# Optimization experiments

Measured on AMD Instinct MI355X. Metric: run time of the kernel, lower is better.

Reference implementation:

```python
import jax, jax.numpy as jnp
import numpy as np

B, S, D, H = 8, 2048, 256, 4
DH = D // H
DFF = 4 * D


def setup_inputs() -> dict:
    key = jax.random.key(0)
    ks = jax.random.split(key, 32)
    w = lambda k, sh: (jax.random.normal(k, sh, jnp.float32) * 0.02)
    inp = {
        'global_feat': jax.random.normal(ks[0], (B, S, D), jnp.float32),
        'local_feat': jax.random.normal(ks[1], (B, S, D), jnp.float32),
        'text_feat': jax.random.normal(ks[2], (B, S, D), jnp.float32),
        'Wl1': w(ks[3], (D, D)), 'bl1': jnp.zeros((D,), jnp.float32),
        'Wl2': w(ks[4], (D, D)), 'bl2': jnp.zeros((D,), jnp.float32),
        'Wg': w(ks[5], (D, D)), 'bg': jnp.zeros((D,), jnp.float32),
        'Wgq': w(ks[6], (D, D)), 'bgq': jnp.zeros((D,), jnp.float32),
        'Wgk': w(ks[7], (D, D)), 'bgk': jnp.zeros((D,), jnp.float32),
        'Wgv': w(ks[8], (D, D)), 'bgv': jnp.zeros((D,), jnp.float32),
        'Wpq': w(ks[9], (D, D)), 'bpq': jnp.zeros((D,), jnp.float32),
        'Wpk': w(ks[10], (D, D)), 'bpk': jnp.zeros((D,), jnp.float32),
        'Wpv': w(ks[11], (D, D)), 'bpv': jnp.zeros((D,), jnp.float32),
        'Wd': w(ks[12], (D, D)), 'bd': jnp.zeros((D,), jnp.float32),
        'Wm1': w(ks[13], (D, DFF)), 'bm1': jnp.zeros((DFF,), jnp.float32),
        'Wm2': w(ks[14], (DFF, D)), 'bm2': jnp.zeros((D,), jnp.float32),
        'Wml': w(ks[15], (D, D)), 'bml': jnp.zeros((D,), jnp.float32),
    }
    return inp


def _heads(x):
    # [B,S,D] -> [B,H,S,DH]
    return x.reshape(B, S, H, DH).transpose(0, 2, 1, 3)


def _merge(x):
    # [B,H,S,DH] -> [B,S,D]
    return x.transpose(0, 2, 1, 3).reshape(B, S, D)


def reference(global_feat, local_feat, text_feat,
              Wl1, bl1, Wl2, bl2, Wg, bg,
              Wgq, bgq, Wgk, bgk, Wgv, bgv,
              Wpq, bpq, Wpk, bpk, Wpv, bpv,
              Wd, bd, Wm1, bm1, Wm2, bm2, Wml, bml):
    scale = 1.0 / jnp.sqrt(jnp.asarray(DH, jnp.float32))
    # embedding projections (dropout inactive in eval mode)
    dup_local = local_feat @ Wl1 + bl1      # local_embedding_1
    local = local_feat @ Wl2 + bl2          # local_embedding_2
    glob = global_feat @ Wg + bg            # global_embedding
    # global branch: Q from global, K/V from local
    gq = _heads(glob @ Wgq + bgq)
    gk = _heads(local @ Wgk + bgk)
    gv = _heads(local @ Wgv + bgv)
    # local branch: Q from duplicate local, K/V from text
    pq = _heads(dup_local @ Wpq + bpq)
    pk = _heads(text_feat @ Wpk + bpk)
    pv = _heads(text_feat @ Wpv + bpv)
    glb_probs = jax.nn.softmax(jnp.einsum('bhqd,bhkd->bhqk', gq, gk) * scale, axis=-1)
    plb_probs = jax.nn.softmax(jnp.einsum('bhqd,bhkd->bhqk', pq, pk) * scale, axis=-1)
    # bridging matmul: fuse probability maps
    plb_enhanced = jnp.einsum('bhqk,bhkl->bhql', glb_probs, plb_probs)
    glb_ctx = _merge(jnp.einsum('bhqk,bhkd->bhqd', glb_probs, gv))
    plb_ctx = _merge(jnp.einsum('bhqk,bhkd->bhqd', plb_enhanced, pv))
    out = (glb_ctx + plb_ctx) @ Wd + bd
    # GPT-style MLP (c_fc -> GELU -> c_proj)
    out = jax.nn.gelu(out @ Wm1 + bm1) @ Wm2 + bm2
    out = out @ Wml + bml
    return out
```

## Files before the change

kernel.cpp:

```cpp
#include <hip/hip_runtime.h>
#include <math.h>

#define Bn 8
#define Sn 2048
#define Dn 256
#define Hn 4
#define DHn 64
#define Mn (Bn*Sn)

typedef short bf16x8 __attribute__((ext_vector_type(8)));
typedef float f32x2  __attribute__((ext_vector_type(2)));
typedef float f32x4  __attribute__((ext_vector_type(4)));
typedef float f32x16 __attribute__((ext_vector_type(16)));
typedef int   i32x4  __attribute__((ext_vector_type(4)));
typedef unsigned short u16;
typedef unsigned int   u32;
typedef unsigned long long u64;

#if defined(__has_builtin)
#if __has_builtin(__builtin_amdgcn_global_load_lds)
#define HAVE_GLL 1
#endif
#if __has_builtin(__builtin_amdgcn_permlane32_swap)
#define HAVE_PLS 1
#endif
#endif
#ifndef HAVE_GLL
#define HAVE_GLL 0
#endif
#ifndef HAVE_PLS
#define HAVE_PLS 0
#endif

__device__ __forceinline__ u16 f2b(float f){
    u32 u = __float_as_uint(f);
    u32 r = (u + 0x7fffu + ((u >> 16) & 1u)) >> 16;
    return (u16)r;
}
__device__ __forceinline__ float b2f(u16 h){ return __uint_as_float(((u32)h) << 16); }
__device__ __forceinline__ u32 cvtpk(float lo, float hi){
    u32 r;
    asm("v_cvt_pk_bf16_f32 %0, %1, %2" : "=v"(r) : "v"(lo), "v"(hi));
    return r;
}

__device__ __forceinline__ float gelu_f(float x){
    const float K1 = 2.3021143113f;
    const float K2 = 0.1029390163f;
    float x2 = x * x;
    float arg = fmaf(x2 * x, K2, x * K1);
    float e = exp2f(arg);
    float r = __builtin_amdgcn_rcpf(e + 1.0f);
    return x - x * r;
}

struct WtArgs {
    const float* src[13];
    int kdim[13], ndim[13], dstoff[13], t0[13], rm[13];
};
struct BcArgs {
    const float* W2[4];
    const float* b1[4];
    const float* b2[4];
    int off[4];
    float* fb;
    int bc0;
};

__global__ __launch_bounds__(256) void prep_k(WtArgs a, u16* __restrict__ dst, BcArgs bc)
{
    __shared__ float tile[32][33];
    int bx = blockIdx.x;
    if (bx >= bc.bc0){
        int p = bx - bc.bc0, aa = threadIdx.x;
        const float* W2 = bc.W2[p];
        const float* b1 = bc.b1[p];
        const float* b2 = bc.b2[p];
        float s = b2[aa];
        for (int j = 0; j < 256; ++j) s = fmaf(b1[j], W2[(size_t)j*256 + aa], s);
        bc.fb[bc.off[p] + aa] = s;
        if (p == 0) bc.fb[1024 + aa] = 0.f;
        return;
    }
    int tb = bx;
    int wi = 0;
    #pragma unroll
    for (int i = 1; i < 13; ++i) if (tb >= a.t0[i]) wi = i;
    int tt = tb - a.t0[wi];
    int N = a.ndim[wi], K = a.kdim[wi];
    int ntn = N >> 5;
    int tn = tt % ntn, tk = tt / ntn;
    int n0 = tn * 32, k0 = tk * 32;
    const float* src = a.src[wi];
    u16* out = dst + a.dstoff[wi];
    int r = threadIdx.x >> 5, c = threadIdx.x & 31;
    if (a.rm[wi]){
        #pragma unroll
        for (int rr = 0; rr < 4; ++rr){
            size_t idx = (size_t)(k0 + r*4 + rr) * N + n0 + c;
            out[idx] = f2b(src[idx]);
        }
        return;
    }
    #pragma unroll
    for (int rr = 0; rr < 4; ++rr)
        tile[r*4+rr][c] = src[(size_t)(k0 + r*4 + rr) * N + n0 + c];
    __syncthreads();
    #pragma unroll
    for (int rr = 0; rr < 4; ++rr)
        out[(size_t)(n0 + r*4 + rr) * K + k0 + c] = f2b(tile[c][r*4+rr]);
}

struct Grp {
    const u16* A[6];
    const u16* Wt[6];
    const float* bias[6];
    void* C[6];
    float scale[6];
};

template<int ACT, int OUTF32>
__global__ __launch_bounds__(256, 4) void gemm_k(Grp g, int N, int K)
{
    const u32 gx = gridDim.x, gy = gridDim.y;
    const u32 lgx = (u32)__builtin_ctz(gx);
    const u32 lgy = (u32)__builtin_ctz(gy);
    const u32 total = gx * gy * gridDim.z;
    const u32 lid = (blockIdx.z * gy + blockIdx.y) * gx + blockIdx.x;
    const u32 nl = (lid & 7) * (total >> 3) + (lid >> 3);
    const u32 bz = nl >> (lgx + lgy);
    const u32 by = (nl >> lgx) & (gy - 1);
    const u32 bx = nl & (gx - 1);

    const u16* __restrict__ A   = g.A[bz];
    const u16* __restrict__ Wt  = g.Wt[bz];
    const float* __restrict__ bias = g.bias[bz];
    void* __restrict__ Cv = g.C[bz];
    const float scale = g.scale[bz];

    __shared__ u16 sm[2][6144];
    const int tid = threadIdx.x;
    const int w = tid >> 6, lane = tid & 63;
    const int l15 = lane & 15, l4 = lane >> 4;
    const int wr = w & 1, wc = w >> 1;
    const int bm = by << 6, bn = bx << 7;
    const int xq = l4 ^ ((lane >> 1) & 3);

    f32x4 acc[4][2];
    #pragma unroll
    for (int nf = 0; nf < 4; ++nf)
        #pragma unroll
        for (int mf = 0; mf < 2; ++mf){
            acc[nf][mf][0]=0.f; acc[nf][mf][1]=0.f; acc[nf][mf][2]=0.f; acc[nf][mf][3]=0.f;
        }

    auto STAGE = [&](int buf, int kt){
        #pragma unroll
        for (int j = 0; j < 3; ++j){
            int ch = w*192 + j*64 + lane;
            int isB = ch >= 256;
            int cc  = isB ? ch - 256 : ch;
            int row = cc >> 2, q = cc & 3;
            int qs  = q ^ ((row >> 1) & 3);
            const u16* src = isB ? (Wt + (size_t)(bn + row) * K + kt + qs*8)
                                 : (A  + (size_t)(bm + row) * K + kt + qs*8);
#if HAVE_GLL
            u16* lb = &sm[buf][(size_t)(w*192 + j*64) * 8];
            __builtin_amdgcn_global_load_lds((const __attribute__((address_space(1))) void*)src,
                                             (__attribute__((address_space(3))) void*)lb, 16, 0, 0);
#else
            *(i32x4*)&sm[buf][(size_t)ch * 8] = *(const i32x4*)src;
#endif
        }
    };

    STAGE(0, 0);
    const int nk = K >> 5;
    for (int t = 0; t < nk; ++t){
        const int cur = t & 1;
        if (t + 1 < nk){
            STAGE(cur ^ 1, (t + 1) << 5);
#if HAVE_GLL
            asm volatile("s_waitcnt vmcnt(3)" ::: "memory");
#endif
        } else {
#if HAVE_GLL
            asm volatile("s_waitcnt vmcnt(0)" ::: "memory");
#endif
        }
        __builtin_amdgcn_s_barrier();
        asm volatile("" ::: "memory");

        const u16* As = sm[cur];
        const u16* Bs = sm[cur] + 2048;
        bf16x8 wf[4], af[2];
        #pragma unroll
        for (int nf = 0; nf < 4; ++nf)
            wf[nf] = *(const bf16x8*)(Bs + (size_t)(wc*64 + nf*16 + l15) * 32 + xq*8);
        #pragma unroll
        for (int mf = 0; mf < 2; ++mf)
            af[mf] = *(const bf16x8*)(As + (size_t)(wr*32 + mf*16 + l15) * 32 + xq*8);
        __builtin_amdgcn_s_setprio(1);
        #pragma unroll
        for (int nf = 0; nf < 4; ++nf)
            #pragma unroll
            for (int mf = 0; mf < 2; ++mf)
                acc[nf][mf] = __builtin_amdgcn_mfma_f32_16x16x32_bf16(wf[nf], af[mf], acc[nf][mf], 0, 0, 0);
        __builtin_amdgcn_s_setprio(0);

        asm volatile("" ::: "memory");
        __builtin_amdgcn_s_barrier();
    }

    #pragma unroll
    for (int nf = 0; nf < 4; ++nf){
        const int n0 = bn + wc*64 + nf*16 + l4*4;
        float4 b4 = *(const float4*)(bias + n0);
        #pragma unroll
        for (int mf = 0; mf < 2; ++mf){
            const int m = bm + wr*32 + mf*16 + l15;
            float r0 = (acc[nf][mf][0] + b4.x) * scale;
            float r1 = (acc[nf][mf][1] + b4.y) * scale;
            float r2 = (acc[nf][mf][2] + b4.z) * scale;
            float r3 = (acc[nf][mf][3] + b4.w) * scale;
            if (ACT){ r0 = gelu_f(r0); r1 = gelu_f(r1); r2 = gelu_f(r2); r3 = gelu_f(r3); }
            if (OUTF32){
                float4 o; o.x = r0; o.y = r1; o.z = r2; o.w = r3;
                *(float4*)((float*)Cv + (size_t)m * N + n0) = o;
            } else {
                u64 p = (u64)cvtpk(r0, r1) | ((u64)cvtpk(r2, r3) << 32);
                *(u64*)((u16*)Cv + (size_t)m * N + n0) = p;
            }
        }
    }
}

struct Grp32 {
    const float* A[6];
    const u16* Wt[6];
    const float* bias[6];
    void* C[6];
    float scale[6];
};

__global__ __launch_bounds__(256, 4) void gemm32_k(Grp32 g, int N, int K)
{
    const u32 gx = gridDim.x, gy = gridDim.y;
    const u32 lgx = (u32)__builtin_ctz(gx);
    const u32 lgy = (u32)__builtin_ctz(gy);
    const u32 total = gx * gy * gridDim.z;
    const u32 lid = (blockIdx.z * gy + blockIdx.y) * gx + blockIdx.x;
    const u32 nl = (lid & 7) * (total >> 3) + (lid >> 3);
    const u32 bz = nl >> (lgx + lgy);
    const u32 by = (nl >> lgx) & (gy - 1);
    const u32 bx = nl & (gx - 1);

    const float* __restrict__ A = g.A[bz];
    const u16* __restrict__ Wt  = g.Wt[bz];
    const float* __restrict__ bias = g.bias[bz];
    void* __restrict__ Cv = g.C[bz];
    const float scale = g.scale[bz];

    __shared__ u16 sm[2][6144];
    const int tid = threadIdx.x;
    const int w = tid >> 6, lane = tid & 63;
    const int l15 = lane & 15, l4 = lane >> 4;
    const int wr = w & 1, wc = w >> 1;
    const int bm = by << 6, bn = bx << 7;
    const int xq = l4 ^ ((lane >> 1) & 3);

    f32x4 acc[4][2];
    #pragma unroll
    for (int nf = 0; nf < 4; ++nf)
        #pragma unroll
        for (int mf = 0; mf < 2; ++mf){
            acc[nf][mf][0]=0.f; acc[nf][mf][1]=0.f; acc[nf][mf][2]=0.f; acc[nf][mf][3]=0.f;
        }

    const int arow = tid >> 2, aq = tid & 3;
    const int aqs = aq ^ ((arow >> 1) & 3);
    const float* Ab = A + (size_t)(bm + arow) * K + aqs*8;
    float4 a0r, a1r;
    auto A_ISSUE = [&](int kt){
        a0r = *(const float4*)(Ab + kt);
        a1r = *(const float4*)(Ab + kt + 4);
    };
    auto A_WRITE = [&](int buf){
        i32x4 o;
        o[0] = (int)cvtpk(a0r.x, a0r.y); o[1] = (int)cvtpk(a0r.z, a0r.w);
        o[2] = (int)cvtpk(a1r.x, a1r.y); o[3] = (int)cvtpk(a1r.z, a1r.w);
        *(i32x4*)&sm[buf][(size_t)tid * 8] = o;
    };
    auto B_STAGE = [&](int buf, int kt){
        #pragma unroll
        for (int j = 0; j < 2; ++j){
            int ch = w*128 + j*64 + lane;
            int row = ch >> 2, q = ch & 3;
            int qs  = q ^ ((row >> 1) & 3);
            const u16* src = Wt + (size_t)(bn + row) * K + kt + qs*8;
#if HAVE_GLL
            u16* lb = &sm[buf][2048 + (size_t)(w*128 + j*64) * 8];
            __builtin_amdgcn_global_load_lds((const __attribute__((address_space(1))) void*)src,
                                             (__attribute__((address_space(3))) void*)lb, 16, 0, 0);
#else
            *(i32x4*)&sm[buf][2048 + (size_t)ch * 8] = *(const i32x4*)src;
#endif
        }
    };

    A_ISSUE(0);
    B_STAGE(0, 0);
    A_WRITE(0);
    __syncthreads();

    const int nk = K >> 5;
    for (int t = 0; t < nk; ++t){
        const int cur = t & 1;
        if (t + 1 < nk){
            A_ISSUE((t + 1) << 5);
            B_STAGE(cur ^ 1, (t + 1) << 5);
#if HAVE_GLL
            asm volatile("s_waitcnt vmcnt(4)" ::: "memory");
#endif
        } else {
#if HAVE_GLL
            asm volatile("s_waitcnt vmcnt(0)" ::: "memory");
#endif
        }
        __builtin_amdgcn_s_barrier();
        asm volatile("" ::: "memory");

        const u16* As = sm[cur];
        const u16* Bs = sm[cur] + 2048;
        bf16x8 wf[4], af[2];
        #pragma unroll
        for (int nf = 0; nf < 4; ++nf)
            wf[nf] = *(const bf16x8*)(Bs + (size_t)(wc*64 + nf*16 + l15) * 32 + xq*8);
        #pragma unroll
        for (int mf = 0; mf < 2; ++mf)
            af[mf] = *(const bf16x8*)(As + (size_t)(wr*32 + mf*16 + l15) * 32 + xq*8);
        __builtin_amdgcn_s_setprio(1);
        #pragma unroll
        for (int nf = 0; nf < 4; ++nf)
            #pragma unroll
            for (int mf = 0; mf < 2; ++mf)
                acc[nf][mf] = __builtin_amdgcn_mfma_f32_16x16x32_bf16(wf[nf], af[mf], acc[nf][mf], 0, 0, 0);
        __builtin_amdgcn_s_setprio(0);

        if (t + 1 < nk) A_WRITE(cur ^ 1);
        asm volatile("" ::: "memory");
        asm volatile("s_waitcnt lgkmcnt(0)" ::: "memory");
        __builtin_amdgcn_s_barrier();
    }

    #pragma unroll
    for (int nf = 0; nf < 4; ++nf){
        const int n0 = bn + wc*64 + nf*16 + l4*4;
        float4 b4 = *(const float4*)(bias + n0);
        #pragma unroll
        for (int mf = 0; mf < 2; ++mf){
            const int m = bm + wr*32 + mf*16 + l15;
            float r0 = (acc[nf][mf][0] + b4.x) * scale;
            float r1 = (acc[nf][mf][1] + b4.y) * scale;
            float r2 = (acc[nf][mf][2] + b4.z) * scale;
            float r3 = (acc[nf][mf][3] + b4.w) * scale;
            u64 p = (u64)cvtpk(r0, r1) | ((u64)cvtpk(r2, r3) << 32);
            *(u64*)((u16*)Cv + (size_t)m * N + n0) = p;
        }
    }
}

template<int FUSE>
__global__ __launch_bounds__(256, 2) void attn_k(const u16* __restrict__ Q, const u16* __restrict__ Kp,
                                                 const u16* __restrict__ Vp, u16* __restrict__ O,
                                                 const u16* __restrict__ ADD)
{
    __shared__ u16 Kl[2][2][4608];
    __shared__ u16 Vt[2][2][4608];

    const int tid = threadIdx.x;
    const int w = tid >> 6, lane = tid & 63;
    const int c31 = lane & 31, h = lane >> 5;

    const int lid = blockIdx.x;
    const int nl = (lid & 7) * 64 + (lid >> 3);
    const int bh = nl >> 4;
    const int qb = (nl & 15) << 7;
    const size_t hb = (size_t)(bh >> 2) * Sn * Dn + (size_t)(bh & 3) * DHn;
    const int qrow = qb + w*32 + c31;

    bf16x8 qf[4];
    #pragma unroll
    for (int kc = 0; kc < 4; ++kc)
        qf[kc] = *(const bf16x8*)(Q + hb + (size_t)qrow * Dn + kc*16 + h*8);

    f32x16 ot0, ot1;
    #pragma unroll
    for (int r = 0; r < 16; ++r){ ot0[r] = 0.f; ot1[r] = 0.f; }
    float ll = 0.f;

    int koff0[4], koff1[4];
    #pragma unroll
    for (int kc = 0; kc < 4; ++kc){
        koff0[kc] = c31*72        + kc*16 + h*8;
        koff1[kc] = (32 + c31)*72 + kc*16 + h*8;
    }

    const int krow = tid >> 1, kq = (tid & 1) * 8;
    const int khalf = krow >> 6, krow63 = krow & 63;
    const int vk0 = (tid & 31) * 4, vd0 = (tid >> 5) * 4;
    const int vhalf = vk0 >> 6, vk63 = vk0 & 63;
    const u32 SEL_LO = 0x05040100u, SEL_HI = 0x07060302u;

    i32x4 kr[4];
    u64 va_[4], vb_[4];
    auto LOADKV = [&](int kt2){
        const u16* kb = Kp + hb + (size_t)(kt2 + krow) * Dn + kq;
        kr[0] = *(const i32x4*)(kb);
        kr[1] = *(const i32x4*)(kb + 16);
        kr[2] = *(const i32x4*)(kb + 32);
        kr[3] = *(const i32x4*)(kb + 48);
        const u16* vb = Vp + hb + (size_t)(kt2 + vk0) * Dn + vd0;
        va_[0] = *(const u64*)(vb);             va_[1] = *(const u64*)(vb + Dn);
        va_[2] = *(const u64*)(vb + 2*Dn);      va_[3] = *(const u64*)(vb + 3*Dn);
        vb_[0] = *(const u64*)(vb + 32);        vb_[1] = *(const u64*)(vb + Dn + 32);
        vb_[2] = *(const u64*)(vb + 2*Dn + 32); vb_[3] = *(const u64*)(vb + 3*Dn + 32);
    };
    auto WRITEKV = [&](int buf){
        u16* kd = &Kl[buf][khalf][(size_t)krow63*72 + kq];
        *(i32x4*)(kd)      = kr[0];
        *(i32x4*)(kd + 16) = kr[1];
        *(i32x4*)(kd + 32) = kr[2];
        *(i32x4*)(kd + 48) = kr[3];
        {
            u32 a0 = (u32)va_[0], a1 = (u32)va_[1], a2 = (u32)va_[2], a3 = (u32)va_[3];
            u32 b0 = (u32)(va_[0] >> 32), b1 = (u32)(va_[1] >> 32), b2 = (u32)(va_[2] >> 32), b3 = (u32)(va_[3] >> 32);
            u64 wd0 = (u64)__builtin_amdgcn_perm(a1, a0, SEL_LO) | ((u64)__builtin_amdgcn_perm(a3, a2, SEL_LO) << 32);
            u64 wd1 = (u64)__builtin_amdgcn_perm(a1, a0, SEL_HI) | ((u64)__builtin_amdgcn_perm(a3, a2, SEL_HI) << 32);
            u64 wd2 = (u64)__builtin_amdgcn_perm(b1, b0, SEL_LO) | ((u64)__builtin_amdgcn_perm(b3, b2, SEL_LO) << 32);
            u64 wd3 = (u64)__builtin_amdgcn_perm(b1, b0, SEL_HI) | ((u64)__builtin_amdgcn_perm(b3, b2, SEL_HI) << 32);
            *(u64*)&Vt[buf][vhalf][(size_t)(vd0 + 0)*72 + vk63] = wd0;
            *(u64*)&Vt[buf][vhalf][(size_t)(vd0 + 1)*72 + vk63] = wd1;
            *(u64*)&Vt[buf][vhalf][(size_t)(vd0 + 2)*72 + vk63] = wd2;
            *(u64*)&Vt[buf][vhalf][(size_t)(vd0 + 3)*72 + vk63] = wd3;
        }
        {
            u32 a0 = (u32)vb_[0], a1 = (u32)vb_[1], a2 = (u32)vb_[2], a3 = (u32)vb_[3];
            u32 b0 = (u32)(vb_[0] >> 32), b1 = (u32)(vb_[1] >> 32), b2 = (u32)(vb_[2] >> 32), b3 = (u32)(vb_[3] >> 32);
            u64 wd0 = (u64)__builtin_amdgcn_perm(a1, a0, SEL_LO) | ((u64)__builtin_amdgcn_perm(a3, a2, SEL_LO) << 32);
            u64 wd1 = (u64)__builtin_amdgcn_perm(a1, a0, SEL_HI) | ((u64)__builtin_amdgcn_perm(a3, a2, SEL_HI) << 32);
            u64 wd2 = (u64)__builtin_amdgcn_perm(b1, b0, SEL_LO) | ((u64)__builtin_amdgcn_perm(b3, b2, SEL_LO) << 32);
            u64 wd3 = (u64)__builtin_amdgcn_perm(b1, b0, SEL_HI) | ((u64)__builtin_amdgcn_perm(b3, b2, SEL_HI) << 32);
            *(u64*)&Vt[buf][vhalf][(size_t)(vd0 + 32)*72 + vk63] = wd0;
            *(u64*)&Vt[buf][vhalf][(size_t)(vd0 + 33)*72 + vk63] = wd1;
            *(u64*)&Vt[buf][vhalf][(size_t)(vd0 + 34)*72 + vk63] = wd2;
            *(u64*)&Vt[buf][vhalf][(size_t)(vd0 + 35)*72 + vk63] = wd3;
        }
    };

    LOADKV(0);
    WRITEKV(0);
    __syncthreads();

    for (int t = 0; t < 16; ++t){
        const int c = t & 1;
        const bool more = (t < 15);
        if (more) LOADKV((t + 1) << 7);

        #pragma unroll
        for (int hh = 0; hh < 2; ++hh){
            f32x16 s0, s1;
            #pragma unroll
            for (int r = 0; r < 16; ++r){ s0[r] = 0.f; s1[r] = 0.f; }
            __builtin_amdgcn_s_setprio(1);
            #pragma unroll
            for (int kc = 0; kc < 4; ++kc){
                bf16x8 k0 = *(const bf16x8*)&Kl[c][hh][koff0[kc]];
                bf16x8 k1 = *(const bf16x8*)&Kl[c][hh][koff1[kc]];
                s0 = __builtin_amdgcn_mfma_f32_32x32x16_bf16(k0, qf[kc], s0, 0, 0, 0);
                s1 = __builtin_amdgcn_mfma_f32_32x32x16_bf16(k1, qf[kc], s1, 0, 0, 0);
            }
            __builtin_amdgcn_s_setprio(0);

            f32x2 pp0[8], pp1[8];
            f32x2 rv = {0.f, 0.f};
            #pragma unroll
            for (int r = 0; r < 8; ++r){
                pp0[r][0] = exp2f(s0[2*r]); pp0[r][1] = exp2f(s0[2*r+1]);
                pp1[r][0] = exp2f(s1[2*r]); pp1[r][1] = exp2f(s1[2*r+1]);
                rv += pp0[r];
                rv += pp1[r];
            }
            ll += rv[0] + rv[1];

            __builtin_amdgcn_s_setprio(1);
            #pragma unroll
            for (int kc = 0; kc < 4; ++kc){
                const int iA = 2*kc, iB = 2*kc + 1;
                u32 wA0, wA1, wB0, wB1;
                if (kc < 2){
                    wA0 = cvtpk(pp0[iA*2+0][0], pp0[iA*2+0][1]);
                    wA1 = cvtpk(pp0[iA*2+1][0], pp0[iA*2+1][1]);
                    wB0 = cvtpk(pp0[iB*2+0][0], pp0[iB*2+0][1]);
                    wB1 = cvtpk(pp0[iB*2+1][0], pp0[iB*2+1][1]);
                } else {
                    wA0 = cvtpk(pp1[(iA-4)*2+0][0], pp1[(iA-4)*2+0][1]);
                    wA1 = cvtpk(pp1[(iA-4)*2+1][0], pp1[(iA-4)*2+1][1]);
                    wB0 = cvtpk(pp1[(iB-4)*2+0][0], pp1[(iB-4)*2+0][1]);
                    wB1 = cvtpk(pp1[(iB-4)*2+1][0], pp1[(iB-4)*2+1][1]);
                }
                i32x4 pw;
#if HAVE_PLS
                {
                    auto r02 = __builtin_amdgcn_permlane32_swap((int)wA0, (int)wB0, false, false);
                    auto r13 = __builtin_amdgcn_permlane32_swap((int)wA1, (int)wB1, false, false);
                    pw[0] = r02[0]; pw[1] = r13[0]; pw[2] = r02[1]; pw[3] = r13[1];
                }
#else
                {
                    u32 s0v = h ? wA0 : wB0, s1v = h ? wA1 : wB1;
                    u32 g0 = (u32)__shfl_xor((int)s0v, 32);
                    u32 g1 = (u32)__shfl_xor((int)s1v, 32);
                    pw[0] = (int)(h ? g0 : wA0);
                    pw[1] = (int)(h ? g1 : wA1);
                    pw[2] = (int)(h ? wB0 : g0);
                    pw[3] = (int)(h ? wB1 : g1);
                }
#endif
                bf16x8 pb = *(bf16x8*)&pw;
                bf16x8 va  = *(const bf16x8*)&Vt[c][hh][koff0[kc]];
                bf16x8 vb2 = *(const bf16x8*)&Vt[c][hh][koff1[kc]];
                ot0 = __builtin_amdgcn_mfma_f32_32x32x16_bf16(va,  pb, ot0, 0, 0, 0);
                ot1 = __builtin_amdgcn_mfma_f32_32x32x16_bf16(vb2, pb, ot1, 0, 0, 0);
            }
            __builtin_amdgcn_s_setprio(0);
        }

        if (more) WRITEKV(c ^ 1);
        __syncthreads();
    }

    ll += __shfl_xor(ll, 32);
    float inv = 1.0f / ll;
    #pragma unroll
    for (int rg = 0; rg < 4; ++rg){
        int d0 = 8*rg + 4*h;
        float r0 = ot0[4*rg+0]*inv, r1 = ot0[4*rg+1]*inv, r2 = ot0[4*rg+2]*inv, r3 = ot0[4*rg+3]*inv;
        float x0 = ot1[4*rg+0]*inv, x1 = ot1[4*rg+1]*inv, x2 = ot1[4*rg+2]*inv, x3 = ot1[4*rg+3]*inv;
        if (FUSE){
            u64 ga = *(const u64*)&ADD[hb + (size_t)qrow * Dn + d0];
            u64 gb = *(const u64*)&ADD[hb + (size_t)qrow * Dn + 32 + d0];
            r0 += b2f((u16)ga);         r1 += b2f((u16)(ga >> 16));
            r2 += b2f((u16)(ga >> 32)); r3 += b2f((u16)(ga >> 48));
            x0 += b2f((u16)gb);         x1 += b2f((u16)(gb >> 16));
            x2 += b2f((u16)(gb >> 32)); x3 += b2f((u16)(gb >> 48));
        }
        *(u64*)&O[hb + (size_t)qrow * Dn + d0]      = (u64)cvtpk(r0, r1) | ((u64)cvtpk(r2, r3) << 32);
        *(u64*)&O[hb + (size_t)qrow * Dn + 32 + d0] = (u64)cvtpk(x0, x1) | ((u64)cvtpk(x2, x3) << 32);
    }
}

extern "C" void kernel_launch(void* const* d_in, const int* in_sizes, int n_in,
                              void* d_out, int out_size, void* d_ws, size_t ws_size,
                              hipStream_t stream)
{
    (void)in_sizes; (void)n_in; (void)out_size; (void)ws_size;

    const float* gf  = (const float*)d_in[0];
    const float* lf  = (const float*)d_in[1];
    const float* tf  = (const float*)d_in[2];
    const float* Wl1 = (const float*)d_in[3];  const float* bl1 = (const float*)d_in[4];
    const float* Wl2 = (const float*)d_in[5];  const float* bl2 = (const float*)d_in[6];
    const float* Wg  = (const float*)d_in[7];  const float* bg  = (const float*)d_in[8];
    const float* Wgq = (const float*)d_in[9];  const float* bgq = (const float*)d_in[10];
    const float* Wgk = (const float*)d_in[11]; const float* bgk = (const float*)d_in[12];
    const float* Wgv = (const float*)d_in[13]; const float* bgv = (const float*)d_in[14];
    const float* Wpq = (const float*)d_in[15]; const float* bpq = (const float*)d_in[16];
    const float* bpk = (const float*)d_in[18];
    const float* bpv = (const float*)d_in[20];
    const float* bd  = (const float*)d_in[22];
    const float* bm1 = (const float*)d_in[24];
    const float* bm2 = (const float*)d_in[26];
    const float* Wml = (const float*)d_in[27]; const float* bml = (const float*)d_in[28];

    const float C1 = 0.18033688011112042f;

    u16* ws = (u16*)d_ws;
    const size_t U = (size_t)Mn * Dn;
    u16* S[9];
    for (int i = 0; i < 9; ++i) S[i] = ws + (size_t)i * U;
    u16* wtb = ws + 9 * U;

    const int sq = 65536;
    u16* Wpqt = wtb + 0*sq;  u16* Wgqt = wtb + 1*sq;  u16* Wgkt = wtb + 2*sq;  u16* Wgvt = wtb + 3*sq;
    u16* Wpkt = wtb + 4*sq;  u16* Wpvt = wtb + 5*sq;  u16* Wdt  = wtb + 6*sq;  u16* Wmlt = wtb + 7*sq;
    u16* Wm1t  = wtb + 524288;
    u16* Wm2t  = wtb + 786432;
    u16* Wl1rm = wtb + 1048576;
    u16* Wl2rm = wtb + 1114112;
    u16* Wgrm  = wtb + 1179648;
    u16* Wcpqt = wtb + 1245184;
    u16* Wcgqt = wtb + 1310720;
    u16* Wcgkt = wtb + 1376256;
    u16* Wcgvt = wtb + 1441792;
    float* fb  = (float*)(wtb + 1507328);

    WtArgs wa;
    const float* wsrc[13] = {Wpq, Wgq, Wgk, Wgv, (const float*)d_in[17], (const float*)d_in[19],
                             (const float*)d_in[21], Wml,
                             (const float*)d_in[23], (const float*)d_in[25], Wl1, Wl2, Wg};
    const int wdst[13] = {0, sq, 2*sq, 3*sq, 4*sq, 5*sq, 6*sq, 7*sq, 524288, 786432,
                          1048576, 1114112, 1179648};
    for (int i = 0; i < 13; ++i){
        wa.src[i] = wsrc[i];
        wa.kdim[i] = 256; wa.ndim[i] = 256;
        wa.dstoff[i] = wdst[i];
        wa.rm[i] = (i >= 10);
    }
    wa.ndim[8] = 1024;
    wa.kdim[9] = 1024;
    int acc_t = 0;
    for (int i = 0; i < 13; ++i){
        wa.t0[i] = acc_t;
        acc_t += (wa.ndim[i] >> 5) * (wa.kdim[i] >> 5);
    }
    BcArgs bc;
    bc.W2[0] = Wpq; bc.W2[1] = Wgq; bc.W2[2] = Wgk; bc.W2[3] = Wgv;
    bc.b1[0] = bl1; bc.b1[1] = bg;  bc.b1[2] = bl2; bc.b1[3] = bl2;
    bc.b2[0] = bpq; bc.b2[1] = bgq; bc.b2[2] = bgk; bc.b2[3] = bgv;
    bc.off[0] = 0; bc.off[1] = 256; bc.off[2] = 512; bc.off[3] = 768;
    bc.fb = fb; bc.bc0 = acc_t;
    prep_k<<<dim3(acc_t + 4), 256, 0, stream>>>(wa, wtb, bc);

    auto GN = [&](const Grp& g, int ng, int M, int N, int K, int act, int of32){
        dim3 gr(N / 128, M / 64, ng);
        if (act)        gemm_k<1,0><<<gr, 256, 0, stream>>>(g, N, K);
        else if (of32)  gemm_k<0,1><<<gr, 256, 0, stream>>>(g, N, K);
        else            gemm_k<0,0><<<gr, 256, 0, stream>>>(g, N, K);
    };
    auto G1 = [&](const u16* A, const u16* Wt_, const float* b, void* C, int M, int N, int K,
                  float sc, int act, int of32){
        Grp g{};
        g.A[0] = A; g.Wt[0] = Wt_; g.bias[0] = b; g.C[0] = C; g.scale[0] = sc;
        GN(g, 1, M, N, K, act, of32);
    };

    {
        Grp g{};
        g.A[0] = Wpqt; g.Wt[0] = Wl1rm; g.bias[0] = fb + 1024; g.C[0] = Wcpqt; g.scale[0] = 1.f;
        g.A[1] = Wgqt; g.Wt[1] = Wgrm;  g.bias[1] = fb + 1024; g.C[1] = Wcgqt; g.scale[1] = 1.f;
        g.A[2] = Wgkt; g.Wt[2] = Wl2rm; g.bias[2] = fb + 1024; g.C[2] = Wcgkt; g.scale[2] = 1.f;
        g.A[3] = Wgvt; g.Wt[3] = Wl2rm; g.bias[3] = fb + 1024; g.C[3] = Wcgvt; g.scale[3] = 1.f;
        GN(g, 4, 256, 256, 256, 0, 0);
    }

    {
        Grp32 g{};
        g.A[0] = lf; g.Wt[0] = Wcpqt; g.bias[0] = fb + 0;   g.C[0] = S[3]; g.scale[0] = C1;
        g.A[1] = gf; g.Wt[1] = Wcgqt; g.bias[1] = fb + 256; g.C[1] = S[6]; g.scale[1] = C1;
        g.A[2] = lf; g.Wt[2] = Wcgkt; g.bias[2] = fb + 512; g.C[2] = S[7]; g.scale[2] = 1.f;
        g.A[3] = lf; g.Wt[3] = Wcgvt; g.bias[3] = fb + 768; g.C[3] = S[8]; g.scale[3] = 1.f;
        g.A[4] = tf; g.Wt[4] = Wpkt;  g.bias[4] = bpk;      g.C[4] = S[4]; g.scale[4] = 1.f;
        g.A[5] = tf; g.Wt[5] = Wpvt;  g.bias[5] = bpv;      g.C[5] = S[5]; g.scale[5] = 1.f;
        dim3 gr(2, Mn / 64, 6);
        gemm32_k<<<gr, 256, 0, stream>>>(g, 256, 256);
    }

    attn_k<1><<<dim3(512), 256, 0, stream>>>(S[3], S[4], S[5], S[0], S[8]);
    attn_k<0><<<dim3(512), 256, 0, stream>>>(S[6], S[7], S[0], S[1], nullptr);

    G1(S[1], Wdt,  bd,  S[2],  Mn, 256,  256,  1.f, 0, 0);
    G1(S[2], Wm1t, bm1, S[3],  Mn, 1024, 256,  1.f, 1, 0);
    G1(S[3], Wm2t, bm2, S[7],  Mn, 256,  1024, 1.f, 0, 0);
    G1(S[7], Wmlt, bml, d_out, Mn, 256,  256,  1.f, 0, 1);
}
```

Measured before the change: 232.7 us.

## Halve attention KV tile to 64 rows with two-stage register prefetch pipeline

The attention kernel's LDS staging changes from 128-key tiles (two 64-row halves per buffer) to 64-key tiles, halving shared memory per block. Loads for the next tile are split into two register sets (A/B) that alternate around compute, with a barrier after every 64-key step instead of every 128. The smaller LDS footprint could allow more resident blocks, at the cost of twice as many barriers and less work between them. The barrier is now a raw s_barrier after waiting only on lgkmcnt, which relies on the LDS writes having completed.

```diff
diff --git a/kernel.cpp b/kernel.cpp
--- a/kernel.cpp
+++ b/kernel.cpp
@@ -375,8 +375,8 @@
                                                  const u16* __restrict__ Vp, u16* __restrict__ O,
                                                  const u16* __restrict__ ADD)
 {
-    __shared__ u16 Kl[2][2][4608];
-    __shared__ u16 Vt[2][2][4608];
+    __shared__ u16 Kl[2][4608];
+    __shared__ u16 Vt[2][4608];
 
     const int tid = threadIdx.x;
     const int w = tid >> 6, lane = tid & 63;
@@ -406,138 +406,151 @@
         koff1[kc] = (32 + c31)*72 + kc*16 + h*8;
     }
 
-    const int krow = tid >> 1, kq = (tid & 1) * 8;
-    const int khalf = krow >> 6, krow63 = krow & 63;
-    const int vk0 = (tid & 31) * 4, vd0 = (tid >> 5) * 4;
-    const int vhalf = vk0 >> 6, vk63 = vk0 & 63;
+    const int krow = tid >> 2, kq = tid & 3;
+    const int vk0 = (tid & 15) * 4, vd0 = (tid >> 4) * 4;
     const u32 SEL_LO = 0x05040100u, SEL_HI = 0x07060302u;
 
-    i32x4 kr[4];
-    u64 va_[4], vb_[4];
-    auto LOADKV = [&](int kt2){
-        const u16* kb = Kp + hb + (size_t)(kt2 + krow) * Dn + kq;
-        kr[0] = *(const i32x4*)(kb);
-        kr[1] = *(const i32x4*)(kb + 16);
-        kr[2] = *(const i32x4*)(kb + 32);
-        kr[3] = *(const i32x4*)(kb + 48);
+    i32x4 krA0, krA1, krB0, krB1;
+    u64 vA0, vA1, vA2, vA3, vB0, vB1, vB2, vB3;
+
+    auto LOADA = [&](int kt2){
+        const u16* kb = Kp + hb + (size_t)(kt2 + krow) * Dn + kq*8;
+        krA0 = *(const i32x4*)kb;
+        krA1 = *(const i32x4*)(kb + 32);
         const u16* vb = Vp + hb + (size_t)(kt2 + vk0) * Dn + vd0;
-        va_[0] = *(const u64*)(vb);             va_[1] = *(const u64*)(vb + Dn);
-        va_[2] = *(const u64*)(vb + 2*Dn);      va_[3] = *(const u64*)(vb + 3*Dn);
-        vb_[0] = *(const u64*)(vb + 32);        vb_[1] = *(const u64*)(vb + Dn + 32);
-        vb_[2] = *(const u64*)(vb + 2*Dn + 32); vb_[3] = *(const u64*)(vb + 3*Dn + 32);
-    };
-    auto WRITEKV = [&](int buf){
-        u16* kd = &Kl[buf][khalf][(size_t)krow63*72 + kq];
-        *(i32x4*)(kd)      = kr[0];
-        *(i32x4*)(kd + 16) = kr[1];
-        *(i32x4*)(kd + 32) = kr[2];
-        *(i32x4*)(kd + 48) = kr[3];
-        {
-            u32 a0 = (u32)va_[0], a1 = (u32)va_[1], a2 = (u32)va_[2], a3 = (u32)va_[3];
-            u32 b0 = (u32)(va_[0] >> 32), b1 = (u32)(va_[1] >> 32), b2 = (u32)(va_[2] >> 32), b3 = (u32)(va_[3] >> 32);
-            u64 wd0 = (u64)__builtin_amdgcn_perm(a1, a0, SEL_LO) | ((u64)__builtin_amdgcn_perm(a3, a2, SEL_LO) << 32);
-            u64 wd1 = (u64)__builtin_amdgcn_perm(a1, a0, SEL_HI) | ((u64)__builtin_amdgcn_perm(a3, a2, SEL_HI) << 32);
-            u64 wd2 = (u64)__builtin_amdgcn_perm(b1, b0, SEL_LO) | ((u64)__builtin_amdgcn_perm(b3, b2, SEL_LO) << 32);
-            u64 wd3 = (u64)__builtin_amdgcn_perm(b1, b0, SEL_HI) | ((u64)__builtin_amdgcn_perm(b3, b2, SEL_HI) << 32);
-            *(u64*)&Vt[buf][vhalf][(size_t)(vd0 + 0)*72 + vk63] = wd0;
-            *(u64*)&Vt[buf][vhalf][(size_t)(vd0 + 1)*72 + vk63] = wd1;
-            *(u64*)&Vt[buf][vhalf][(size_t)(vd0 + 2)*72 + vk63] = wd2;
-            *(u64*)&Vt[buf][vhalf][(size_t)(vd0 + 3)*72 + vk63] = wd3;
-        }
-        {
-            u32 a0 = (u32)vb_[0], a1 = (u32)vb_[1], a2 = (u32)vb_[2], a3 = (u32)vb_[3];
-            u32 b0 = (u32)(vb_[0] >> 32), b1 = (u32)(vb_[1] >> 32), b2 = (u32)(vb_[2] >> 32), b3 = (u32)(vb_[3] >> 32);
-            u64 wd0 = (u64)__builtin_amdgcn_perm(a1, a0, SEL_LO) | ((u64)__builtin_amdgcn_perm(a3, a2, SEL_LO) << 32);
-            u64 wd1 = (u64)__builtin_amdgcn_perm(a1, a0, SEL_HI) | ((u64)__builtin_amdgcn_perm(a3, a2, SEL_HI) << 32);
-            u64 wd2 = (u64)__builtin_amdgcn_perm(b1, b0, SEL_LO) | ((u64)__builtin_amdgcn_perm(b3, b2, SEL_LO) << 32);
-            u64 wd3 = (u64)__builtin_amdgcn_perm(b1, b0, SEL_HI) | ((u64)__builtin_amdgcn_perm(b3, b2, SEL_HI) << 32);
-            *(u64*)&Vt[buf][vhalf][(size_t)(vd0 + 32)*72 + vk63] = wd0;
-            *(u64*)&Vt[buf][vhalf][(size_t)(vd0 + 33)*72 + vk63] = wd1;
-            *(u64*)&Vt[buf][vhalf][(size_t)(vd0 + 34)*72 + vk63] = wd2;
-            *(u64*)&Vt[buf][vhalf][(size_t)(vd0 + 35)*72 + vk63] = wd3;
-        }
-    };
-
-    LOADKV(0);
-    WRITEKV(0);
-    __syncthreads();
-
-    for (int t = 0; t < 16; ++t){
-        const int c = t & 1;
-        const bool more = (t < 15);
-        if (more) LOADKV((t + 1) << 7);
-
-        #pragma unroll
-        for (int hh = 0; hh < 2; ++hh){
-            f32x16 s0, s1;
-            #pragma unroll
-            for (int r = 0; r < 16; ++r){ s0[r] = 0.f; s1[r] = 0.f; }
-            __builtin_amdgcn_s_setprio(1);
-            #pragma unroll
-            for (int kc = 0; kc < 4; ++kc){
-                bf16x8 k0 = *(const bf16x8*)&Kl[c][hh][koff0[kc]];
-                bf16x8 k1 = *(const bf16x8*)&Kl[c][hh][koff1[kc]];
-                s0 = __builtin_amdgcn_mfma_f32_32x32x16_bf16(k0, qf[kc], s0, 0, 0, 0);
-                s1 = __builtin_amdgcn_mfma_f32_32x32x16_bf16(k1, qf[kc], s1, 0, 0, 0);
+        vA0 = *(const u64*)(vb);
+        vA1 = *(const u64*)(vb + Dn);
+        vA2 = *(const u64*)(vb + 2*Dn);
+        vA3 = *(const u64*)(vb + 3*Dn);
+    };
+    auto LOADB = [&](int kt2){
+        const u16* kb = Kp + hb + (size_t)(kt2 + krow) * Dn + kq*8;
+        krB0 = *(const i32x4*)kb;
+        krB1 = *(const i32x4*)(kb + 32);
+        const u16* vb = Vp + hb + (size_t)(kt2 + vk0) * Dn + vd0;
+        vB0 = *(const u64*)(vb);
+        vB1 = *(const u64*)(vb + Dn);
+        vB2 = *(const u64*)(vb + 2*Dn);
+        vB3 = *(const u64*)(vb + 3*Dn);
+    };
+    auto WRITEA = [&](int buf){
+        *(i32x4*)&Kl[buf][(size_t)krow*72 + kq*8]      = krA0;
+        *(i32x4*)&Kl[buf][(size_t)krow*72 + kq*8 + 32] = krA1;
+        u32 a0 = (u32)vA0, a1 = (u32)vA1, a2 = (u32)vA2, a3 = (u32)vA3;
+        u32 b0 = (u32)(vA0 >> 32), b1 = (u32)(vA1 >> 32), b2 = (u32)(vA2 >> 32), b3 = (u32)(vA3 >> 32);
+        u64 wd0 = (u64)__builtin_amdgcn_perm(a1, a0, SEL_LO) | ((u64)__builtin_amdgcn_perm(a3, a2, SEL_LO) << 32);
+        u64 wd1 = (u64)__builtin_amdgcn_perm(a1, a0, SEL_HI) | ((u64)__builtin_amdgcn_perm(a3, a2, SEL_HI) << 32);
+        u64 wd2 = (u64)__builtin_amdgcn_perm(b1, b0, SEL_LO) | ((u64)__builtin_amdgcn_perm(b3, b2, SEL_LO) << 32);
+        u64 wd3 = (u64)__builtin_amdgcn_perm(b1, b0, SEL_HI) | ((u64)__builtin_amdgcn_perm(b3, b2, SEL_HI) << 32);
+        *(u64*)&Vt[buf][(size_t)(vd0 + 0)*72 + vk0] = wd0;
+        *(u64*)&Vt[buf][(size_t)(vd0 + 1)*72 + vk0] = wd1;
+        *(u64*)&Vt[buf][(size_t)(vd0 + 2)*72 + vk0] = wd2;
+        *(u64*)&Vt[buf][(size_t)(vd0 + 3)*72 + vk0] = wd3;
+    };
+    auto WRITEB = [&](int buf){
+        *(i32x4*)&Kl[buf][(size_t)krow*72 + kq*8]      = krB0;
+        *(i32x4*)&Kl[buf][(size_t)krow*72 + kq*8 + 32] = krB1;
+        u32 a0 = (u32)vB0, a1 = (u32)vB1, a2 = (u32)vB2, a3 = (u32)vB3;
+        u32 b0 = (u32)(vB0 >> 32), b1 = (u32)(vB1 >> 32), b2 = (u32)(vB2 >> 32), b3 = (u32)(vB3 >> 32);
+        u64 wd0 = (u64)__builtin_amdgcn_perm(a1, a0, SEL_LO) | ((u64)__builtin_amdgcn_perm(a3, a2, SEL_LO) << 32);
+        u64 wd1 = (u64)__builtin_amdgcn_perm(a1, a0, SEL_HI) | ((u64)__builtin_amdgcn_perm(a3, a2, SEL_HI) << 32);
+        u64 wd2 = (u64)__builtin_amdgcn_perm(b1, b0, SEL_LO) | ((u64)__builtin_amdgcn_perm(b3, b2, SEL_LO) << 32);
+        u64 wd3 = (u64)__builtin_amdgcn_perm(b1, b0, SEL_HI) | ((u64)__builtin_amdgcn_perm(b3, b2, SEL_HI) << 32);
+        *(u64*)&Vt[buf][(size_t)(vd0 + 0)*72 + vk0] = wd0;
+        *(u64*)&Vt[buf][(size_t)(vd0 + 1)*72 + vk0] = wd1;
+        *(u64*)&Vt[buf][(size_t)(vd0 + 2)*72 + vk0] = wd2;
+        *(u64*)&Vt[buf][(size_t)(vd0 + 3)*72 + vk0] = wd3;
+    };
+
+    auto COMPUTE = [&](int c){
+        f32x16 s0, s1;
+        #pragma unroll
+        for (int r = 0; r < 16; ++r){ s0[r] = 0.f; s1[r] = 0.f; }
+        __builtin_amdgcn_s_setprio(1);
+        #pragma unroll
+        for (int kc = 0; kc < 4; ++kc){
+            bf16x8 k0 = *(const bf16x8*)&Kl[c][koff0[kc]];
+            bf16x8 k1 = *(const bf16x8*)&Kl[c][koff1[kc]];
+            s0 = __builtin_amdgcn_mfma_f32_32x32x16_bf16(k0, qf[kc], s0, 0, 0, 0);
+            s1 = __builtin_amdgcn_mfma_f32_32x32x16_bf16(k1, qf[kc], s1, 0, 0, 0);
+        }
+        __builtin_amdgcn_s_setprio(0);
+
+        f32x2 pp0[8], pp1[8];
+        f32x2 rv = {0.f, 0.f};
+        #pragma unroll
+        for (int r = 0; r < 8; ++r){
+            pp0[r][0] = exp2f(s0[2*r]); pp0[r][1] = exp2f(s0[2*r+1]);
+            pp1[r][0] = exp2f(s1[2*r]); pp1[r][1] = exp2f(s1[2*r+1]);
+            rv += pp0[r];
+            rv += pp1[r];
+        }
+        ll += rv[0] + rv[1];
+
+        __builtin_amdgcn_s_setprio(1);
+        #pragma unroll
+        for (int kc = 0; kc < 4; ++kc){
+            const int iA = 2*kc, iB = 2*kc + 1;
+            u32 wA0, wA1, wB0, wB1;
+            if (kc < 2){
+                wA0 = cvtpk(pp0[iA*2+0][0], pp0[iA*2+0][1]);
+                wA1 = cvtpk(pp0[iA*2+1][0], pp0[iA*2+1][1]);
+                wB0 = cvtpk(pp0[iB*2+0][0], pp0[iB*2+0][1]);
+                wB1 = cvtpk(pp0[iB*2+1][0], pp0[iB*2+1][1]);
+            } else {
+                wA0 = cvtpk(pp1[(iA-4)*2+0][0], pp1[(iA-4)*2+0][1]);
+                wA1 = cvtpk(pp1[(iA-4)*2+1][0], pp1[(iA-4)*2+1][1]);
+                wB0 = cvtpk(pp1[(iB-4)*2+0][0], pp1[(iB-4)*2+0][1]);
+                wB1 = cvtpk(pp1[(iB-4)*2+1][0], pp1[(iB-4)*2+1][1]);
             }
-            __builtin_amdgcn_s_setprio(0);
-
-            f32x2 pp0[8], pp1[8];
-            f32x2 rv = {0.f, 0.f};
-            #pragma unroll
-            for (int r = 0; r < 8; ++r){
-                pp0[r][0] = exp2f(s0[2*r]); pp0[r][1] = exp2f(s0[2*r+1]);
-                pp1[r][0] = exp2f(s1[2*r]); pp1[r][1] = exp2f(s1[2*r+1]);
-                rv += pp0[r];
-                rv += pp1[r];
+            i32x4 pw;
+#if HAVE_PLS
+            {
+                auto r02 = __builtin_amdgcn_permlane32_swap((int)wA0, (int)wB0, false, false);
+                auto r13 = __builtin_amdgcn_permlane32_swap((int)wA1, (int)wB1, false, false);
+                pw[0] = r02[0]; pw[1] = r13[0]; pw[2] = r02[1]; pw[3] = r13[1];
             }
-            ll += rv[0] + rv[1];
-
-            __builtin_amdgcn_s_setprio(1);
-            #pragma unroll
-            for (int kc = 0; kc < 4; ++kc){
-                const int iA = 2*kc, iB = 2*kc + 1;
-                u32 wA0, wA1, wB0, wB1;
-                if (kc < 2){
-                    wA0 = cvtpk(pp0[iA*2+0][0], pp0[iA*2+0][1]);
-                    wA1 = cvtpk(pp0[iA*2+1][0], pp0[iA*2+1][1]);
-                    wB0 = cvtpk(pp0[iB*2+0][0], pp0[iB*2+0][1]);
-                    wB1 = cvtpk(pp0[iB*2+1][0], pp0[iB*2+1][1]);
-                } else {
-                    wA0 = cvtpk(pp1[(iA-4)*2+0][0], pp1[(iA-4)*2+0][1]);
-                    wA1 = cvtpk(pp1[(iA-4)*2+1][0], pp1[(iA-4)*2+1][1]);
-                    wB0 = cvtpk(pp1[(iB-4)*2+0][0], pp1[(iB-4)*2+0][1]);
-                    wB1 = cvtpk(pp1[(iB-4)*2+1][0], pp1[(iB-4)*2+1][1]);
-                }
-                i32x4 pw;
-#if HAVE_PLS
-                {
-                    auto r02 = __builtin_amdgcn_permlane32_swap((int)wA0, (int)wB0, false, false);
-                    auto r13 = __builtin_amdgcn_permlane32_swap((int)wA1, (int)wB1, false, false);
-                    pw[0] = r02[0]; pw[1] = r13[0]; pw[2] = r02[1]; pw[3] = r13[1];
-                }
 #else
-                {
-                    u32 s0v = h ? wA0 : wB0, s1v = h ? wA1 : wB1;
-                    u32 g0 = (u32)__shfl_xor((int)s0v, 32);
-                    u32 g1 = (u32)__shfl_xor((int)s1v, 32);
-                    pw[0] = (int)(h ? g0 : wA0);
-                    pw[1] = (int)(h ? g1 : wA1);
-                    pw[2] = (int)(h ? wB0 : g0);
-                    pw[3] = (int)(h ? wB1 : g1);
-                }
-#endif
-                bf16x8 pb = *(bf16x8*)&pw;
-                bf16x8 va  = *(const bf16x8*)&Vt[c][hh][koff0[kc]];
-                bf16x8 vb2 = *(const bf16x8*)&Vt[c][hh][koff1[kc]];
-                ot0 = __builtin_amdgcn_mfma_f32_32x32x16_bf16(va,  pb, ot0, 0, 0, 0);
-                ot1 = __builtin_amdgcn_mfma_f32_32x32x16_bf16(vb2, pb, ot1, 0, 0, 0);
+            {
+                u32 s0v = h ? wA0 : wB0, s1v = h ? wA1 : wB1;
+                u32 g0 = (u32)__shfl_xor((int)s0v, 32);
+                u32 g1 = (u32)__shfl_xor((int)s1v, 32);
+                pw[0] = (int)(h ? g0 : wA0);
+                pw[1] = (int)(h ? g1 : wA1);
+                pw[2] = (int)(h ? wB0 : g0);
+                pw[3] = (int)(h ? wB1 : g1);
             }
-            __builtin_amdgcn_s_setprio(0);
-        }
-
-        if (more) WRITEKV(c ^ 1);
-        __syncthreads();
+#endif
+            bf16x8 pb = *(bf16x8*)&pw;
+            bf16x8 va  = *(const bf16x8*)&Vt[c][koff0[kc]];
+            bf16x8 vb2 = *(const bf16x8*)&Vt[c][koff1[kc]];
+            ot0 = __builtin_amdgcn_mfma_f32_32x32x16_bf16(va,  pb, ot0, 0, 0, 0);
+            ot1 = __builtin_amdgcn_mfma_f32_32x32x16_bf16(vb2, pb, ot1, 0, 0, 0);
+        }
+        __builtin_amdgcn_s_setprio(0);
+    };
+
+    LOADA(0);
+    WRITEA(0);
+    LOADB(1 << 6);
+    asm volatile("s_waitcnt lgkmcnt(0)" ::: "memory");
+    __builtin_amdgcn_s_barrier();
+    asm volatile("" ::: "memory");
+
+    for (int tp = 0; tp < 16; ++tp){
+        if (tp < 15) LOADA((2*tp + 2) << 6);
+        COMPUTE(0);
+        WRITEB(1);
+        asm volatile("s_waitcnt lgkmcnt(0)" ::: "memory");
+        __builtin_amdgcn_s_barrier();
+        asm volatile("" ::: "memory");
+
+        if (tp < 15) LOADB((2*tp + 3) << 6);
+        COMPUTE(1);
+        if (tp < 15) WRITEA(0);
+        asm volatile("s_waitcnt lgkmcnt(0)" ::: "memory");
+        __builtin_amdgcn_s_barrier();
+        asm volatile("" ::: "memory");
     }
 
     ll += __shfl_xor(ll, 32);
```

Result: faster. 218.3 us (-6.2%).
